# Kernel tuning notes

Hardware: AMD Instinct MI355X
Metric: run time of the kernel (lower is better)

The kernel has to match this reference:

```python
import jax, jax.numpy as jnp
import numpy as np

N_EMBD = 1024
N_HEAD = 16
HEAD_SIZE = 64
BLOCK_SIZE = 2048


def setup_inputs() -> dict:
    key = jax.random.key(0)
    ks = jax.random.split(key, 5)
    B, T = 2, 2048
    s_attn = 1.0 / np.sqrt(N_EMBD)
    x = jax.random.normal(ks[0], (B, T, N_EMBD), dtype=jnp.float32)
    W_attn = jax.random.normal(ks[1], (N_EMBD, 3 * N_EMBD), dtype=jnp.float32) * s_attn
    b_attn = jnp.zeros((3 * N_EMBD,), dtype=jnp.float32)
    W_proj = jax.random.normal(ks[2], (N_EMBD, N_EMBD), dtype=jnp.float32) * s_attn
    b_proj = jnp.zeros((N_EMBD,), dtype=jnp.float32)
    return {"x": x, "W_attn": W_attn, "b_attn": b_attn, "W_proj": W_proj, "b_proj": b_proj}


def reference(x, W_attn, b_attn, W_proj, b_proj):
    B, T, C = x.shape
    H, D = N_HEAD, HEAD_SIZE
    qkv = x @ W_attn + b_attn                      # [B, T, 3C]
    q, k, v = jnp.split(qkv, 3, axis=-1)
    # [B, H, T, D]
    q = q.reshape(B, T, H, D).transpose(0, 2, 1, 3)
    k = k.reshape(B, T, H, D).transpose(0, 2, 1, 3)
    v = v.reshape(B, T, H, D).transpose(0, 2, 1, 3)
    scores = jnp.einsum("bhqd,bhkd->bhqk", q, k) / jnp.sqrt(jnp.float32(D))
    causal = jnp.tril(jnp.ones((T, T), dtype=bool))
    scores = jnp.where(causal[None, None, :, :], scores, -jnp.inf)
    weights = jax.nn.softmax(scores, axis=-1)
    attn = jnp.einsum("bhqk,bhkd->bhqd", weights, v)  # [B, H, T, D]
    attn = attn.transpose(0, 2, 1, 3).reshape(B, T, C)
    return attn @ W_proj + b_proj
```

## Files before the change

kernel.cpp:

```cpp
#include <hip/hip_runtime.h>
#include <hip/hip_bf16.h>

#define NE 1024
#define NH 16
#define HD 64
#define TSEQ 2048
#define BATCH 2
#define MB (1024u * 1024u)

typedef __attribute__((ext_vector_type(8))) short bf16x8;
typedef __attribute__((ext_vector_type(4))) float f32x4;
typedef __attribute__((ext_vector_type(4))) unsigned int u32x4;
typedef unsigned short u16;
typedef unsigned int u32;

__device__ inline u16 f2bf(float f) {
    __hip_bfloat16 h = __float2bfloat16(f);
    return *reinterpret_cast<u16*>(&h);
}

__device__ inline float bf2f(u32 bits) {
    u32 v = bits << 16;
    return __builtin_bit_cast(float, v);
}

__device__ inline u32 cvt_pk_bf16(float lo, float hi) {
    u32 r;
    asm("v_cvt_pk_bf16_f32 %0, %1, %2" : "=v"(r) : "v"(lo), "v"(hi));
    return r;
}

#define GLD16(gptr, lptr)                                                        \
    __builtin_amdgcn_global_load_lds(                                            \
        (const __attribute__((address_space(1))) void*)(gptr),                   \
        (__attribute__((address_space(3))) void*)(lptr), 16, 0, 0)

__global__ void k_f32_to_bf16(const float* __restrict__ in, u16* __restrict__ out, int n4) {
    int i = blockIdx.x * blockDim.x + threadIdx.x;
    int stride = gridDim.x * blockDim.x;
    for (; i < n4; i += stride) {
        float4 v = reinterpret_cast<const float4*>(in)[i];
        ushort4 o;
        o.x = f2bf(v.x); o.y = f2bf(v.y); o.z = f2bf(v.z); o.w = f2bf(v.w);
        reinterpret_cast<ushort4*>(out)[i] = o;
    }
}

__global__ void k_prep_w(const float* __restrict__ Wa, const float* __restrict__ Wp,
                         u16* __restrict__ WaT, u16* __restrict__ WpT) {
    __shared__ float tile[32][33];
    const bool isA = blockIdx.x < 96;
    const float* in = isA ? Wa : Wp;
    u16* out = isA ? WaT : WpT;
    const int N = isA ? 3 * NE : NE;
    const int K = NE;
    int bn = (isA ? blockIdx.x : blockIdx.x - 96) * 32;
    int bk = blockIdx.y * 32;
    int tx = threadIdx.x, ty = threadIdx.y;
#pragma unroll
    for (int i = 0; i < 32; i += 8)
        tile[ty + i][tx] = in[(size_t)(bk + ty + i) * N + bn + tx];
    __syncthreads();
#pragma unroll
    for (int i = 0; i < 32; i += 8)
        out[(size_t)(bn + ty + i) * K + bk + tx] = f2bf(tile[tx][ty + i]);
}

template <int MODE>
__global__ __launch_bounds__(256, 2) void k_gemm_bt(
    const u16* __restrict__ A, const u16* __restrict__ Bt,
    const float* __restrict__ bias, void* __restrict__ outp,
    int M, int N, int K) {
    __shared__ __align__(16) u16 As[2][128 * 32];
    __shared__ __align__(16) u16 Bs[2][128 * 32];
    const int l = threadIdx.x & 63;
    const int w = threadIdx.x >> 6;
    const int m0 = blockIdx.x * 128;
    const int n0 = blockIdx.y * 128;
    const int wr = w >> 1, wc = w & 1;
    const int srow = l >> 2;
    const int scol = (l & 3) * 8;

    f32x4 acc[4][4] = {};
    const int nkt = K >> 5;

#pragma unroll
    for (int i = 0; i < 2; ++i) {
        int c = w * 2 + i;
        GLD16(A + (size_t)(m0 + c * 16 + srow) * K + scol, &As[0][c * 512]);
        GLD16(Bt + (size_t)(n0 + c * 16 + srow) * K + scol, &Bs[0][c * 512]);
    }
    __syncthreads();

    int cur = 0;
    for (int kt = 0; kt < nkt; ++kt) {
        if (kt + 1 < nkt) {
            int nb = cur ^ 1;
            int kc = ((kt + 1) << 5) + scol;
#pragma unroll
            for (int i = 0; i < 2; ++i) {
                int c = w * 2 + i;
                GLD16(A + (size_t)(m0 + c * 16 + srow) * K + kc, &As[nb][c * 512]);
                GLD16(Bt + (size_t)(n0 + c * 16 + srow) * K + kc, &Bs[nb][c * 512]);
            }
        }
        bf16x8 af[4], bfr[4];
#pragma unroll
        for (int mi = 0; mi < 4; ++mi)
            af[mi] = *reinterpret_cast<const bf16x8*>(
                &As[cur][(wr * 64 + mi * 16 + (l & 15)) * 32 + (l >> 4) * 8]);
#pragma unroll
        for (int ni = 0; ni < 4; ++ni)
            bfr[ni] = *reinterpret_cast<const bf16x8*>(
                &Bs[cur][(wc * 64 + ni * 16 + (l & 15)) * 32 + (l >> 4) * 8]);
#pragma unroll
        for (int mi = 0; mi < 4; ++mi)
#pragma unroll
            for (int ni = 0; ni < 4; ++ni)
                acc[mi][ni] = __builtin_amdgcn_mfma_f32_16x16x32_bf16(af[mi], bfr[ni], acc[mi][ni], 0, 0, 0);
        __syncthreads();
        cur ^= 1;
    }

    if (MODE == 1) {
        float* C = (float*)outp;
#pragma unroll
        for (int mi = 0; mi < 4; ++mi)
#pragma unroll
            for (int ni = 0; ni < 4; ++ni) {
                int n = n0 + wc * 64 + ni * 16 + (l & 15);
                float bv = bias[n];
#pragma unroll
                for (int r = 0; r < 4; ++r) {
                    int m = m0 + wr * 64 + mi * 16 + (l >> 4) * 4 + r;
                    C[(size_t)m * N + n] = acc[mi][ni][r] + bv;
                }
            }
    } else {
        u16* qkv = (u16*)outp;
        const size_t headsz = (size_t)BATCH * NH * TSEQ * HD;
#pragma unroll
        for (int mi = 0; mi < 4; ++mi)
#pragma unroll
            for (int ni = 0; ni < 4; ++ni) {
                int n = n0 + wc * 64 + ni * 16 + (l & 15);
                float bv = bias[n];
                int which = n >> 10;
                int c = n & 1023;
                int h = c >> 6, d = c & 63;
#pragma unroll
                for (int r = 0; r < 4; ++r) {
                    int m = m0 + wr * 64 + mi * 16 + (l >> 4) * 4 + r;
                    int b = m >> 11, t = m & 2047;
                    float v = acc[mi][ni][r] + bv;
                    size_t dst;
                    if (which == 2)
                        dst = 2 * headsz + ((size_t)(b * NH + h) * HD + d) * TSEQ + t;
                    else
                        dst = (size_t)which * headsz + ((size_t)(b * NH + h) * TSEQ + t) * HD + d;
                    qkv[dst] = f2bf(v);
                }
            }
    }
}

__global__ __launch_bounds__(256, 4) void k_attn(
    const u16* __restrict__ qb, const u16* __restrict__ kb, const u16* __restrict__ vtb,
    u16* __restrict__ oPart, float* __restrict__ mlPart) {
    __shared__ __align__(16) u16 Ks[2][64 * 64];
    __shared__ __align__(16) u16 Vs[2][64 * 64];
    const int l = threadIdx.x & 63;
    const int w = threadIdx.x >> 6;
    const int g = l >> 4, l15 = l & 15;

    const int bid = blockIdx.x;
    const int t = 31 - (bid >> 6);
    const int half = (bid >> 5) & 1;
    const int bh = bid & 31;
    const int q0 = t * 64;
    const int nA = (t + 2) >> 1;
    const int ktLo = half ? nA : 0;
    const int ktHi = half ? (t + 1) : nA;

    const size_t base = (size_t)bh * TSEQ * HD;
    const u16* Q = qb + base;
    const u16* Kg = kb + base;
    const u16* Vg = vtb + base;

    const int lrow8 = l >> 3;
    const int lchunk = (l & 7) ^ lrow8;

    const int qrow = q0 + w * 16 + l15;
    bf16x8 qa[2];
    qa[0] = *reinterpret_cast<const bf16x8*>(Q + (size_t)qrow * HD + g * 8);
    qa[1] = *reinterpret_cast<const bf16x8*>(Q + (size_t)qrow * HD + 32 + g * 8);

    float mrow = -1e30f;
    f32x4 o[4] = {};
    f32x4 os = {};

    const float SC = 0.125f * 1.44269504f;
    const float THRU = 44.3614f;

    const int srcA = ((2 * g) & 3) * 16 + l15;
    const int srcB = ((2 * g + 1) & 3) * 16 + l15;
    const bool losel = (g < 2);

    u32x4 onesw = {0x3F803F80u, 0x3F803F80u, 0x3F803F80u, 0x3F803F80u};
    const bf16x8 onesA = __builtin_bit_cast(bf16x8, onesw);

    if (ktLo < ktHi) {
#pragma unroll
        for (int i2 = 0; i2 < 2; ++i2) {
            int c = w * 2 + i2;
            GLD16(Kg + (size_t)(ktLo * 64 + c * 8 + lrow8) * HD + lchunk * 8, &Ks[0][c * 512]);
            GLD16(Vg + (size_t)(c * 8 + lrow8) * TSEQ + ktLo * 64 + lchunk * 8, &Vs[0][c * 512]);
        }
        __syncthreads();

        int cur = 0;
        for (int kt = ktLo; kt < ktHi; ++kt) {
            if (kt + 1 < ktHi) {
                int nb = cur ^ 1;
#pragma unroll
                for (int i2 = 0; i2 < 2; ++i2) {
                    int c = w * 2 + i2;
                    GLD16(Kg + (size_t)((kt + 1) * 64 + c * 8 + lrow8) * HD + lchunk * 8,
                          &Ks[nb][c * 512]);
                    GLD16(Vg + (size_t)(c * 8 + lrow8) * TSEQ + (kt + 1) * 64 + lchunk * 8,
                          &Vs[nb][c * 512]);
                }
            }
            const u16* Kc = Ks[cur];
            const u16* Vc = Vs[cur];

            f32x4 s[4] = {};
            __builtin_amdgcn_s_setprio(1);
#pragma unroll
            for (int f = 0; f < 4; ++f)
#pragma unroll
                for (int ks = 0; ks < 2; ++ks) {
                    bf16x8 bk = *reinterpret_cast<const bf16x8*>(
                        Kc + (f * 16 + l15) * 64 + (((ks * 4 + g) ^ (l15 & 7)) * 8));
                    s[f] = __builtin_amdgcn_mfma_f32_16x16x32_bf16(bk, qa[ks], s[f], 0, 0, 0);
                }
            __builtin_amdgcn_s_setprio(0);

            if (kt == t) {
#pragma unroll
                for (int f = 0; f < 4; ++f)
#pragma unroll
                    for (int r = 0; r < 4; ++r) {
                        int kg = (kt << 6) + f * 16 + g * 4 + r;
                        if (kg > qrow) s[f][r] = -1e30f;
                    }
            }

            float rmax = -1e30f;
#pragma unroll
            for (int f = 0; f < 4; ++f)
                rmax = fmaxf(rmax, fmaxf(fmaxf(s[f][0], s[f][1]), fmaxf(s[f][2], s[f][3])));
            rmax = fmaxf(rmax, __shfl_xor(rmax, 16));
            rmax = fmaxf(rmax, __shfl_xor(rmax, 32));

            if (__any(rmax - mrow > THRU)) {
                float mnew = fmaxf(mrow, rmax);
                float alpha = exp2f((mrow - mnew) * SC);
                mrow = mnew;
#pragma unroll
                for (int r = 0; r < 4; ++r)
                    os[r] *= alpha;
#pragma unroll
                for (int nf = 0; nf < 4; ++nf)
#pragma unroll
                    for (int r = 0; r < 4; ++r)
                        o[nf][r] *= alpha;
            }
            const float mc = mrow * SC;

            u32 w0[4], w1[4];
#pragma unroll
            for (int f = 0; f < 4; ++f) {
                float p0 = exp2f(__builtin_fmaf(s[f][0], SC, -mc));
                float p1 = exp2f(__builtin_fmaf(s[f][1], SC, -mc));
                float p2 = exp2f(__builtin_fmaf(s[f][2], SC, -mc));
                float p3 = exp2f(__builtin_fmaf(s[f][3], SC, -mc));
                w0[f] = cvt_pk_bf16(p0, p1);
                w1[f] = cvt_pk_bf16(p2, p3);
            }

            __builtin_amdgcn_s_setprio(1);
#pragma unroll
            for (int ks = 0; ks < 2; ++ks) {
                u32 t00 = (u32)__shfl((int)w0[2 * ks], srcA);
                u32 t01 = (u32)__shfl((int)w0[2 * ks + 1], srcA);
                u32 t10 = (u32)__shfl((int)w1[2 * ks], srcA);
                u32 t11 = (u32)__shfl((int)w1[2 * ks + 1], srcA);
                u32 t20 = (u32)__shfl((int)w0[2 * ks], srcB);
                u32 t21 = (u32)__shfl((int)w0[2 * ks + 1], srcB);
                u32 t30 = (u32)__shfl((int)w1[2 * ks], srcB);
                u32 t31 = (u32)__shfl((int)w1[2 * ks + 1], srcB);
                u32x4 bb;
                bb.x = losel ? t00 : t01;
                bb.y = losel ? t10 : t11;
                bb.z = losel ? t20 : t21;
                bb.w = losel ? t30 : t31;
                bf16x8 pb = __builtin_bit_cast(bf16x8, bb);
                os = __builtin_amdgcn_mfma_f32_16x16x32_bf16(onesA, pb, os, 0, 0, 0);
#pragma unroll
                for (int nf = 0; nf < 4; ++nf) {
                    bf16x8 bv = *reinterpret_cast<const bf16x8*>(
                        Vc + (nf * 16 + l15) * 64 + (((ks * 4 + g) ^ (l15 & 7)) * 8));
                    o[nf] = __builtin_amdgcn_mfma_f32_16x16x32_bf16(bv, pb, o[nf], 0, 0, 0);
                }
            }
            __builtin_amdgcn_s_setprio(0);
            __syncthreads();
            cur ^= 1;
        }
    }

    const float lsum = os[0];
    const size_t oHalf = (size_t)32 * TSEQ * HD;
    u16* oRow = oPart + half * oHalf + ((size_t)bh * TSEQ + qrow) * HD;
#pragma unroll
    for (int nf = 0; nf < 4; ++nf) {
        int d0 = nf * 16 + g * 4;
        u32 p01 = cvt_pk_bf16(o[nf][0], o[nf][1]);
        u32 p23 = cvt_pk_bf16(o[nf][2], o[nf][3]);
        *reinterpret_cast<u32*>(oRow + d0) = p01;
        *reinterpret_cast<u32*>(oRow + d0 + 2) = p23;
    }
    if (g == 0) {
        float* mlH = mlPart + half * ((size_t)32 * 2 * TSEQ);
        mlH[((size_t)bh * 2 + 0) * TSEQ + qrow] = mrow;
        mlH[((size_t)bh * 2 + 1) * TSEQ + qrow] = lsum;
    }
}

__global__ void k_merge(const u16* __restrict__ oPart, const float* __restrict__ mlPart,
                        u16* __restrict__ attn_out) {
    const float SC = 0.125f * 1.44269504f;
    int tid = blockIdx.x * blockDim.x + threadIdx.x;
    int dblk = tid & 7;
    int q = (tid >> 3) & 2047;
    int bh = tid >> 14;
    const size_t oHalf = (size_t)32 * TSEQ * HD;
    const size_t mlHalf = (size_t)32 * 2 * TSEQ;
    float mA = mlPart[((size_t)bh * 2 + 0) * TSEQ + q];
    float lA = mlPart[((size_t)bh * 2 + 1) * TSEQ + q];
    float mB = mlPart[mlHalf + ((size_t)bh * 2 + 0) * TSEQ + q];
    float lB = mlPart[mlHalf + ((size_t)bh * 2 + 1) * TSEQ + q];
    float M = fmaxf(mA, mB);
    float eA = exp2f((mA - M) * SC);
    float eB = exp2f((mB - M) * SC);
    float invL = 1.0f / (lA * eA + lB * eB);
    float fA = eA * invL, fB = eB * invL;
    const u32* pa = (const u32*)(oPart + ((size_t)bh * TSEQ + q) * HD + dblk * 8);
    const u32* pb = (const u32*)(oPart + oHalf + ((size_t)bh * TSEQ + q) * HD + dblk * 8);
    u32 outw[4];
#pragma unroll
    for (int i = 0; i < 4; ++i) {
        u32 a = pa[i], b = pb[i];
        float lo = bf2f(a & 0xffffu) * fA + bf2f(b & 0xffffu) * fB;
        float hi = bf2f(a >> 16) * fA + bf2f(b >> 16) * fB;
        outw[i] = cvt_pk_bf16(lo, hi);
    }
    int bb = bh >> 4, h = bh & 15;
    u16* dst = attn_out + ((size_t)(bb * TSEQ + q) * NE) + h * HD + dblk * 8;
    *reinterpret_cast<u32x4*>(dst) = *reinterpret_cast<const u32x4*>(outw);
}

extern "C" void kernel_launch(void* const* d_in, const int* in_sizes, int n_in,
                              void* d_out, int out_size, void* d_ws, size_t ws_size,
                              hipStream_t stream) {
    const float* x = (const float*)d_in[0];
    const float* W_attn = (const float*)d_in[1];
    const float* b_attn = (const float*)d_in[2];
    const float* W_proj = (const float*)d_in[3];
    const float* b_proj = (const float*)d_in[4];
    float* out = (float*)d_out;

    char* ws = (char*)d_ws;
    u16* xb     = (u16*)(ws);
    u16* WaT    = (u16*)(ws + 8 * MB);
    u16* qkvb   = (u16*)(ws + 16 * MB);
    u16* attn   = (u16*)(ws + 40 * MB);
    u16* WpT    = (u16*)(ws + 48 * MB);
    float* mlP  = (float*)(ws + 50 * MB);
    u16* oPart  = (u16*)(ws);

    const int M = BATCH * TSEQ;

    k_f32_to_bf16<<<2048, 256, 0, stream>>>(x, xb, (M * NE) / 4);
    k_prep_w<<<dim3(128, NE / 32), dim3(32, 8), 0, stream>>>(W_attn, W_proj, WaT, WpT);

    k_gemm_bt<0><<<dim3(M / 128, (3 * NE) / 128), 256, 0, stream>>>(xb, WaT, b_attn, qkvb, M, 3 * NE, NE);

    const size_t headsz = (size_t)BATCH * NH * TSEQ * HD;
    k_attn<<<dim3(32 * 2 * 32), 256, 0, stream>>>(qkvb, qkvb + headsz, qkvb + 2 * headsz, oPart, mlP);

    k_merge<<<dim3((32 * TSEQ * 8) / 256), 256, 0, stream>>>(oPart, mlP, attn);

    k_gemm_bt<1><<<dim3(M / 128, NE / 128), 256, 0, stream>>>(attn, WpT, b_proj, out, M, NE, NE);
}
```

Measured before the change: 125.3 us.

## Double query rows per attention block to reuse K/V tiles across two query fragments

Each attention block now handles 128 query rows: each wave covers 32 rows as two 16-row MFMA fragments, and the grid is halved. Every K/V tile loaded into LDS therefore feeds twice as many MFMAs, cutting LDS traffic and global K/V loads per unit of work. The two halves now split the key range at t+1 tiles, and the running max starts at zero instead of -1e30. The workspace layout is also reshuffled so attn reuses the qkv region. The trade-off is higher register pressure under launch_bounds(256,4), fewer blocks, and coarser causal load balance.

New measurement: 124.9 us. About the same (-0.3%).

```diff
diff --git a/kernel.cpp b/kernel.cpp
--- a/kernel.cpp
+++ b/kernel.cpp
@@ -174,13 +174,12 @@
     const int g = l >> 4, l15 = l & 15;
 
     const int bid = blockIdx.x;
-    const int t = 31 - (bid >> 6);
+    const int t = 15 - (bid >> 6);
     const int half = (bid >> 5) & 1;
     const int bh = bid & 31;
-    const int q0 = t * 64;
-    const int nA = (t + 2) >> 1;
-    const int ktLo = half ? nA : 0;
-    const int ktHi = half ? (t + 1) : nA;
+    const int q0 = t * 128;
+    const int ktLo = half ? (t + 1) : 0;
+    const int ktHi = half ? (2 * t + 2) : (t + 1);
 
     const size_t base = (size_t)bh * TSEQ * HD;
     const u16* Q = qb + base;
@@ -190,14 +189,18 @@
     const int lrow8 = l >> 3;
     const int lchunk = (l & 7) ^ lrow8;
 
-    const int qrow = q0 + w * 16 + l15;
-    bf16x8 qa[2];
-    qa[0] = *reinterpret_cast<const bf16x8*>(Q + (size_t)qrow * HD + g * 8);
-    qa[1] = *reinterpret_cast<const bf16x8*>(Q + (size_t)qrow * HD + 32 + g * 8);
-
-    float mrow = -1e30f;
-    f32x4 o[4] = {};
-    f32x4 os = {};
+    const int qrow0 = q0 + w * 32 + l15;
+    const int qrow1 = qrow0 + 16;
+    bf16x8 qa[2][2];
+#pragma unroll
+    for (int ks = 0; ks < 2; ++ks) {
+        qa[0][ks] = *reinterpret_cast<const bf16x8*>(Q + (size_t)qrow0 * HD + ks * 32 + g * 8);
+        qa[1][ks] = *reinterpret_cast<const bf16x8*>(Q + (size_t)qrow1 * HD + ks * 32 + g * 8);
+    }
+
+    float m[2] = {0.f, 0.f};
+    f32x4 o[2][4] = {};
+    f32x4 os[2] = {};
 
     const float SC = 0.125f * 1.44269504f;
     const float THRU = 44.3614f;
@@ -209,132 +212,144 @@
     u32x4 onesw = {0x3F803F80u, 0x3F803F80u, 0x3F803F80u, 0x3F803F80u};
     const bf16x8 onesA = __builtin_bit_cast(bf16x8, onesw);
 
-    if (ktLo < ktHi) {
-#pragma unroll
-        for (int i2 = 0; i2 < 2; ++i2) {
-            int c = w * 2 + i2;
-            GLD16(Kg + (size_t)(ktLo * 64 + c * 8 + lrow8) * HD + lchunk * 8, &Ks[0][c * 512]);
-            GLD16(Vg + (size_t)(c * 8 + lrow8) * TSEQ + ktLo * 64 + lchunk * 8, &Vs[0][c * 512]);
-        }
-        __syncthreads();
-
-        int cur = 0;
-        for (int kt = ktLo; kt < ktHi; ++kt) {
-            if (kt + 1 < ktHi) {
-                int nb = cur ^ 1;
-#pragma unroll
-                for (int i2 = 0; i2 < 2; ++i2) {
-                    int c = w * 2 + i2;
-                    GLD16(Kg + (size_t)((kt + 1) * 64 + c * 8 + lrow8) * HD + lchunk * 8,
-                          &Ks[nb][c * 512]);
-                    GLD16(Vg + (size_t)(c * 8 + lrow8) * TSEQ + (kt + 1) * 64 + lchunk * 8,
-                          &Vs[nb][c * 512]);
+#pragma unroll
+    for (int i2 = 0; i2 < 2; ++i2) {
+        int c = w * 2 + i2;
+        GLD16(Kg + (size_t)(ktLo * 64 + c * 8 + lrow8) * HD + lchunk * 8, &Ks[0][c * 512]);
+        GLD16(Vg + (size_t)(c * 8 + lrow8) * TSEQ + ktLo * 64 + lchunk * 8, &Vs[0][c * 512]);
+    }
+    __syncthreads();
+
+    int cur = 0;
+    for (int kt = ktLo; kt < ktHi; ++kt) {
+        if (kt + 1 < ktHi) {
+            int nb = cur ^ 1;
+#pragma unroll
+            for (int i2 = 0; i2 < 2; ++i2) {
+                int c = w * 2 + i2;
+                GLD16(Kg + (size_t)((kt + 1) * 64 + c * 8 + lrow8) * HD + lchunk * 8,
+                      &Ks[nb][c * 512]);
+                GLD16(Vg + (size_t)(c * 8 + lrow8) * TSEQ + (kt + 1) * 64 + lchunk * 8,
+                      &Vs[nb][c * 512]);
+            }
+        }
+        const u16* Kc = Ks[cur];
+        const u16* Vc = Vs[cur];
+
+        f32x4 s[4][2] = {};
+        __builtin_amdgcn_s_setprio(1);
+#pragma unroll
+        for (int f = 0; f < 4; ++f)
+#pragma unroll
+            for (int ks = 0; ks < 2; ++ks) {
+                bf16x8 bk = *reinterpret_cast<const bf16x8*>(
+                    Kc + (f * 16 + l15) * 64 + (((ks * 4 + g) ^ (l15 & 7)) * 8));
+                s[f][0] = __builtin_amdgcn_mfma_f32_16x16x32_bf16(bk, qa[0][ks], s[f][0], 0, 0, 0);
+                s[f][1] = __builtin_amdgcn_mfma_f32_16x16x32_bf16(bk, qa[1][ks], s[f][1], 0, 0, 0);
+            }
+        __builtin_amdgcn_s_setprio(0);
+
+        if (kt >= 2 * t) {
+#pragma unroll
+            for (int f = 0; f < 4; ++f)
+#pragma unroll
+                for (int r = 0; r < 4; ++r) {
+                    int kg = (kt << 6) + f * 16 + g * 4 + r;
+                    if (kg > qrow0) s[f][0][r] = -1e30f;
+                    if (kg > qrow1) s[f][1][r] = -1e30f;
                 }
-            }
-            const u16* Kc = Ks[cur];
-            const u16* Vc = Vs[cur];
-
-            f32x4 s[4] = {};
-            __builtin_amdgcn_s_setprio(1);
+        }
+
+        u32 pk0[2][4], pk1[2][4];
+#pragma unroll
+        for (int qn = 0; qn < 2; ++qn) {
+            float rmax = -1e30f;
 #pragma unroll
             for (int f = 0; f < 4; ++f)
-#pragma unroll
-                for (int ks = 0; ks < 2; ++ks) {
-                    bf16x8 bk = *reinterpret_cast<const bf16x8*>(
-                        Kc + (f * 16 + l15) * 64 + (((ks * 4 + g) ^ (l15 & 7)) * 8));
-                    s[f] = __builtin_amdgcn_mfma_f32_16x16x32_bf16(bk, qa[ks], s[f], 0, 0, 0);
-                }
-            __builtin_amdgcn_s_setprio(0);
-
-            if (kt == t) {
-#pragma unroll
-                for (int f = 0; f < 4; ++f)
-#pragma unroll
-                    for (int r = 0; r < 4; ++r) {
-                        int kg = (kt << 6) + f * 16 + g * 4 + r;
-                        if (kg > qrow) s[f][r] = -1e30f;
-                    }
-            }
-
-            float rmax = -1e30f;
-#pragma unroll
-            for (int f = 0; f < 4; ++f)
-                rmax = fmaxf(rmax, fmaxf(fmaxf(s[f][0], s[f][1]), fmaxf(s[f][2], s[f][3])));
+                rmax = fmaxf(rmax, fmaxf(fmaxf(s[f][qn][0], s[f][qn][1]),
+                                         fmaxf(s[f][qn][2], s[f][qn][3])));
             rmax = fmaxf(rmax, __shfl_xor(rmax, 16));
             rmax = fmaxf(rmax, __shfl_xor(rmax, 32));
 
-            if (__any(rmax - mrow > THRU)) {
-                float mnew = fmaxf(mrow, rmax);
-                float alpha = exp2f((mrow - mnew) * SC);
-                mrow = mnew;
+            if (__any(rmax - m[qn] > THRU)) {
+                float mnew = fmaxf(m[qn], rmax);
+                float alpha = exp2f((m[qn] - mnew) * SC);
+                m[qn] = mnew;
 #pragma unroll
                 for (int r = 0; r < 4; ++r)
-                    os[r] *= alpha;
+                    os[qn][r] *= alpha;
 #pragma unroll
                 for (int nf = 0; nf < 4; ++nf)
 #pragma unroll
                     for (int r = 0; r < 4; ++r)
-                        o[nf][r] *= alpha;
-            }
-            const float mc = mrow * SC;
-
-            u32 w0[4], w1[4];
+                        o[qn][nf][r] *= alpha;
+            }
+            const float mc = m[qn] * SC;
 #pragma unroll
             for (int f = 0; f < 4; ++f) {
-                float p0 = exp2f(__builtin_fmaf(s[f][0], SC, -mc));
-                float p1 = exp2f(__builtin_fmaf(s[f][1], SC, -mc));
-                float p2 = exp2f(__builtin_fmaf(s[f][2], SC, -mc));
-                float p3 = exp2f(__builtin_fmaf(s[f][3], SC, -mc));
-                w0[f] = cvt_pk_bf16(p0, p1);
-                w1[f] = cvt_pk_bf16(p2, p3);
-            }
-
-            __builtin_amdgcn_s_setprio(1);
-#pragma unroll
-            for (int ks = 0; ks < 2; ++ks) {
-                u32 t00 = (u32)__shfl((int)w0[2 * ks], srcA);
-                u32 t01 = (u32)__shfl((int)w0[2 * ks + 1], srcA);
-                u32 t10 = (u32)__shfl((int)w1[2 * ks], srcA);
-                u32 t11 = (u32)__shfl((int)w1[2 * ks + 1], srcA);
-                u32 t20 = (u32)__shfl((int)w0[2 * ks], srcB);
-                u32 t21 = (u32)__shfl((int)w0[2 * ks + 1], srcB);
-                u32 t30 = (u32)__shfl((int)w1[2 * ks], srcB);
-                u32 t31 = (u32)__shfl((int)w1[2 * ks + 1], srcB);
+                float p0 = exp2f(__builtin_fmaf(s[f][qn][0], SC, -mc));
+                float p1 = exp2f(__builtin_fmaf(s[f][qn][1], SC, -mc));
+                float p2 = exp2f(__builtin_fmaf(s[f][qn][2], SC, -mc));
+                float p3 = exp2f(__builtin_fmaf(s[f][qn][3], SC, -mc));
+                pk0[qn][f] = cvt_pk_bf16(p0, p1);
+                pk1[qn][f] = cvt_pk_bf16(p2, p3);
+            }
+        }
+
+        __builtin_amdgcn_s_setprio(1);
+#pragma unroll
+        for (int ks = 0; ks < 2; ++ks) {
+            bf16x8 pb[2];
+#pragma unroll
+            for (int qn = 0; qn < 2; ++qn) {
+                u32 t00 = (u32)__shfl((int)pk0[qn][2 * ks], srcA);
+                u32 t01 = (u32)__shfl((int)pk0[qn][2 * ks + 1], srcA);
+                u32 t10 = (u32)__shfl((int)pk1[qn][2 * ks], srcA);
+                u32 t11 = (u32)__shfl((int)pk1[qn][2 * ks + 1], srcA);
+                u32 t20 = (u32)__shfl((int)pk0[qn][2 * ks], srcB);
+                u32 t21 = (u32)__shfl((int)pk0[qn][2 * ks + 1], srcB);
+                u32 t30 = (u32)__shfl((int)pk1[qn][2 * ks], srcB);
+                u32 t31 = (u32)__shfl((int)pk1[qn][2 * ks + 1], srcB);
                 u32x4 bb;
                 bb.x = losel ? t00 : t01;
                 bb.y = losel ? t10 : t11;
                 bb.z = losel ? t20 : t21;
                 bb.w = losel ? t30 : t31;
-                bf16x8 pb = __builtin_bit_cast(bf16x8, bb);
-                os = __builtin_amdgcn_mfma_f32_16x16x32_bf16(onesA, pb, os, 0, 0, 0);
-#pragma unroll
-                for (int nf = 0; nf < 4; ++nf) {
-                    bf16x8 bv = *reinterpret_cast<const bf16x8*>(
-                        Vc + (nf * 16 + l15) * 64 + (((ks * 4 + g) ^ (l15 & 7)) * 8));
-                    o[nf] = __builtin_amdgcn_mfma_f32_16x16x32_bf16(bv, pb, o[nf], 0, 0, 0);
-                }
-            }
-            __builtin_amdgcn_s_setprio(0);
-            __syncthreads();
-            cur ^= 1;
-        }
-    }
-
-    const float lsum = os[0];
+                pb[qn] = __builtin_bit_cast(bf16x8, bb);
+            }
+            os[0] = __builtin_amdgcn_mfma_f32_16x16x32_bf16(onesA, pb[0], os[0], 0, 0, 0);
+            os[1] = __builtin_amdgcn_mfma_f32_16x16x32_bf16(onesA, pb[1], os[1], 0, 0, 0);
+#pragma unroll
+            for (int nf = 0; nf < 4; ++nf) {
+                bf16x8 bv = *reinterpret_cast<const bf16x8*>(
+                    Vc + (nf * 16 + l15) * 64 + (((ks * 4 + g) ^ (l15 & 7)) * 8));
+                o[0][nf] = __builtin_amdgcn_mfma_f32_16x16x32_bf16(bv, pb[0], o[0][nf], 0, 0, 0);
+                o[1][nf] = __builtin_amdgcn_mfma_f32_16x16x32_bf16(bv, pb[1], o[1][nf], 0, 0, 0);
+            }
+        }
+        __builtin_amdgcn_s_setprio(0);
+        __syncthreads();
+        cur ^= 1;
+    }
+
     const size_t oHalf = (size_t)32 * TSEQ * HD;
-    u16* oRow = oPart + half * oHalf + ((size_t)bh * TSEQ + qrow) * HD;
-#pragma unroll
-    for (int nf = 0; nf < 4; ++nf) {
-        int d0 = nf * 16 + g * 4;
-        u32 p01 = cvt_pk_bf16(o[nf][0], o[nf][1]);
-        u32 p23 = cvt_pk_bf16(o[nf][2], o[nf][3]);
-        *reinterpret_cast<u32*>(oRow + d0) = p01;
-        *reinterpret_cast<u32*>(oRow + d0 + 2) = p23;
-    }
-    if (g == 0) {
-        float* mlH = mlPart + half * ((size_t)32 * 2 * TSEQ);
-        mlH[((size_t)bh * 2 + 0) * TSEQ + qrow] = mrow;
-        mlH[((size_t)bh * 2 + 1) * TSEQ + qrow] = lsum;
+#pragma unroll
+    for (int qn = 0; qn < 2; ++qn) {
+        int qrow = qn ? qrow1 : qrow0;
+        u16* oRow = oPart + half * oHalf + ((size_t)bh * TSEQ + qrow) * HD;
+#pragma unroll
+        for (int nf = 0; nf < 4; ++nf) {
+            int d0 = nf * 16 + g * 4;
+            u32 p01 = cvt_pk_bf16(o[qn][nf][0], o[qn][nf][1]);
+            u32 p23 = cvt_pk_bf16(o[qn][nf][2], o[qn][nf][3]);
+            *reinterpret_cast<u32*>(oRow + d0) = p01;
+            *reinterpret_cast<u32*>(oRow + d0 + 2) = p23;
+        }
+        if (g == 0) {
+            float* mlH = mlPart + half * ((size_t)32 * 2 * TSEQ);
+            mlH[((size_t)bh * 2 + 0) * TSEQ + qrow] = m[qn];
+            mlH[((size_t)bh * 2 + 1) * TSEQ + qrow] = os[qn][0];
+        }
     }
 }
 
@@ -385,10 +400,10 @@
     u16* xb     = (u16*)(ws);
     u16* WaT    = (u16*)(ws + 8 * MB);
     u16* qkvb   = (u16*)(ws + 16 * MB);
-    u16* attn   = (u16*)(ws + 40 * MB);
-    u16* WpT    = (u16*)(ws + 48 * MB);
-    float* mlP  = (float*)(ws + 50 * MB);
+    u16* WpT    = (u16*)(ws + 40 * MB);
+    float* mlP  = (float*)(ws + 42 * MB);
     u16* oPart  = (u16*)(ws);
+    u16* attn   = (u16*)(ws + 16 * MB);
 
     const int M = BATCH * TSEQ;
 
@@ -398,7 +413,7 @@
     k_gemm_bt<0><<<dim3(M / 128, (3 * NE) / 128), 256, 0, stream>>>(xb, WaT, b_attn, qkvb, M, 3 * NE, NE);
 
     const size_t headsz = (size_t)BATCH * NH * TSEQ * HD;
-    k_attn<<<dim3(32 * 2 * 32), 256, 0, stream>>>(qkvb, qkvb + headsz, qkvb + 2 * headsz, oPart, mlP);
+    k_attn<<<dim3(16 * 2 * 32), 256, 0, stream>>>(qkvb, qkvb + headsz, qkvb + 2 * headsz, oPart, mlP);
 
     k_merge<<<dim3((32 * TSEQ * 8) / 256), 256, 0, stream>>>(oPart, mlP, attn);
 
```
